# Performance work log

Measured on AMD Instinct MI355X. Metric: run time of the kernel, lower is better.

The kernel has to match this reference:

```python
import jax, jax.numpy as jnp
import numpy as np

N = 20000      # nodes
E = 640000     # edges (avg degree 32)
H = 128        # hidden_channels
L = 12         # num_layers
DIN = 3        # node feature dim
DE = 4         # edge feature dim
DOUT = 16      # output dim (y_s size)
EPS = 1e-7     # GENConv message eps
LN_EPS = 1e-5


def setup_inputs() -> dict:
    key = jax.random.key(0)
    ks = jax.random.split(key, 12)

    def w(k, shape, fan_in):
        return (jax.random.normal(k, shape, dtype=jnp.float32) / np.float32(np.sqrt(fan_in)))

    return {
        "x": jax.random.normal(ks[0], (N, DIN), dtype=jnp.float32),
        "edge_index": jax.random.randint(ks[1], (2, E), 0, N, dtype=jnp.int32),
        "edge_attr": jax.random.uniform(ks[2], (E, DE), dtype=jnp.float32),
        "enc_node_w": w(ks[3], (DIN, H), DIN),
        "enc_node_b": jnp.zeros((H,), jnp.float32),
        "enc_edge_w": w(ks[4], (DE, H), DE),
        "enc_edge_b": jnp.zeros((H,), jnp.float32),
        "t": jnp.ones((L,), jnp.float32),                 # learnable softmax temperature per layer
        "mlp1_w": w(ks[5], (L, H, 2 * H), H),
        "mlp1_b": jnp.zeros((L, 2 * H), jnp.float32),
        "mlp_ln_g": jnp.ones((L, 2 * H), jnp.float32),
        "mlp_ln_b": jnp.zeros((L, 2 * H), jnp.float32),
        "mlp2_w": w(ks[6], (L, 2 * H, H), 2 * H),
        "mlp2_b": jnp.zeros((L, H), jnp.float32),
        "ln_g": jnp.ones((L, H), jnp.float32),            # DeepGCNLayer pre-norm params
        "ln_b": jnp.zeros((L, H), jnp.float32),
        "lin_w": w(ks[7], (H, DOUT), H),
        "lin_b": jnp.zeros((DOUT,), jnp.float32),
    }


def _layer_norm(x, g, b):
    mu = jnp.mean(x, axis=-1, keepdims=True)
    var = jnp.mean(jnp.square(x - mu), axis=-1, keepdims=True)
    return (x - mu) * jax.lax.rsqrt(var + LN_EPS) * g + b


def _genconv(h, src, dst, ea, ti, w1, b1, g1, bb1, w2, b2):
    # message: relu(x_j + edge_attr) + eps  -> [E, H]
    m = jax.nn.relu(h[src] + ea) + EPS
    # learnable-temperature softmax over edges grouped by destination node
    logits = m * ti
    mx = jax.ops.segment_max(logits, dst, num_segments=N)
    mx = jnp.where(jnp.isfinite(mx), mx, 0.0)  # guard empty segments
    ex = jnp.exp(logits - mx[dst])
    den = jax.ops.segment_sum(ex, dst, num_segments=N) + 1e-16
    agg = jax.ops.segment_sum(m * (ex / den[dst]), dst, num_segments=N)
    # GENConv update: out = MLP(agg + x) with MLP = Lin(H,2H)->LN->ReLU->Lin(2H,H)
    out = agg + h
    u = jax.nn.relu(_layer_norm(out @ w1 + b1, g1, bb1))
    return u @ w2 + b2


def reference(x, edge_index, edge_attr, enc_node_w, enc_node_b, enc_edge_w,
              enc_edge_b, t, mlp1_w, mlp1_b, mlp_ln_g, mlp_ln_b, mlp2_w,
              mlp2_b, ln_g, ln_b, lin_w, lin_b):
    src, dst = edge_index[0], edge_index[1]
    h = x @ enc_node_w + enc_node_b            # node encoder
    ea = edge_attr @ enc_edge_w + enc_edge_b   # edge encoder

    # first layer: conv only (no norm/act, no residual)
    h = _genconv(h, src, dst, ea, t[0], mlp1_w[0], mlp1_b[0], mlp_ln_g[0],
                 mlp_ln_b[0], mlp2_w[0], mlp2_b[0])

    # remaining layers: res+ block  x = x + conv(relu(norm(x)))
    for i in range(1, L):
        hn = jax.nn.relu(_layer_norm(h, ln_g[i], ln_b[i]))
        h = h + _genconv(hn, src, dst, ea, t[i], mlp1_w[i], mlp1_b[i],
                         mlp_ln_g[i], mlp_ln_b[i], mlp2_w[i], mlp2_b[i])

    # final: layers[0].act(layers[0].norm(x)) then output linear
    h = jax.nn.relu(_layer_norm(h, ln_g[0], ln_b[0]))
    return h @ lin_w + lin_b
```

## Files before the change

### kernel.cpp

```cpp
#include <hip/hip_runtime.h>
#include <hip/hip_bf16.h>
#include <math.h>

#define NN 20000
#define EE 640000
#define HH 128
#define LL 12
#define DOUT_ 16
#define EPS_ 1e-7f
#define LN_EPS_ 1e-5f

typedef unsigned short u16;
typedef unsigned int u32;
typedef __attribute__((ext_vector_type(8))) short bf16x8;
typedef __attribute__((ext_vector_type(4))) float f32x4;

__device__ inline u16 bf16_rne(float v) {
  u32 u = __float_as_uint(v);
  return (u16)((u + 0x7FFFu + ((u >> 16) & 1u)) >> 16);
}
__device__ inline float bf16_tof(u16 h) { return __uint_as_float(((u32)h) << 16); }

__global__ __launch_bounds__(256) void hist_kernel(const int* __restrict__ dst, int* __restrict__ deg) {
  int e = blockIdx.x * 256 + threadIdx.x;
  if (e < EE) atomicAdd(&deg[dst[e]], 1);
}

__global__ __launch_bounds__(1024) void scan_kernel(const int* __restrict__ deg, int* __restrict__ off,
                                                    int* __restrict__ cur) {
  __shared__ int part[1024];
  int tid = threadIdx.x;
  const int CH = (NN + 1023) >> 10;
  int base = tid * CH;
  int s = 0;
  for (int j = 0; j < CH; ++j) { int i = base + j; if (i < NN) s += deg[i]; }
  part[tid] = s;
  __syncthreads();
  for (int d = 1; d < 1024; d <<= 1) {
    int v = (tid >= d) ? part[tid - d] : 0;
    __syncthreads();
    part[tid] += v;
    __syncthreads();
  }
  int run = part[tid] - s;
  for (int j = 0; j < CH; ++j) {
    int i = base + j;
    if (i < NN) { off[i] = run; cur[i] = run; run += deg[i]; }
  }
  if (tid == 1023) off[NN] = part[1023];
}

__global__ __launch_bounds__(256) void scatter_kernel(const int* __restrict__ src, const int* __restrict__ dst,
                                                      const float4* __restrict__ ea, int* __restrict__ cur,
                                                      int* __restrict__ srcs, float4* __restrict__ ea4) {
  int e = blockIdx.x * 256 + threadIdx.x;
  if (e >= EE) return;
  int d = dst[e];
  int p = atomicAdd(&cur[d], 1);
  srcs[p] = src[e];
  ea4[p] = ea[e];
}

__global__ __launch_bounds__(256) void wpack_kernel(const float* __restrict__ w, u16* __restrict__ dh,
                                                    int K, int N, int KSC) {
  int fid = blockIdx.x * 256 + threadIdx.x;
  int perL = (K * N) >> 3;
  if (fid >= LL * perL) return;
  int l = fid / perL, r = fid % perL;
  int lane = r & 63;
  int r2 = r >> 6;
  int ks2 = r2 % KSC; r2 /= KSC;
  int NT = N >> 4;
  int tI = r2 % NT;
  int chunk = r2 / NT;
  int c16 = lane & 15, kg = lane >> 4;
  int n = tI * 16 + c16;
  int k0 = (chunk * KSC + ks2) * 32 + kg * 8;
  const float* ws = w + (size_t)l * K * N;
  u16* oh = dh + (size_t)fid * 8;
  #pragma unroll
  for (int j = 0; j < 8; ++j) {
    oh[j] = bf16_rne(ws[(size_t)(k0 + j) * N + n]);
  }
}

__global__ __launch_bounds__(256) void encoder_kernel(const float* __restrict__ x, const float* __restrict__ w,
                                                      const float* __restrict__ b, float* __restrict__ h,
                                                      u16* __restrict__ hb) {
  int id = blockIdx.x * 256 + threadIdx.x;
  if (id >= NN * 64) return;
  int n = id >> 6, cp = id & 63;
  int c0 = cp * 2;
  float x0 = x[n*3+0], x1 = x[n*3+1], x2 = x[n*3+2];
  float vx = b[c0]   + x0*w[c0]   + x1*w[HH+c0]   + x2*w[2*HH+c0];
  float vy = b[c0+1] + x0*w[c0+1] + x1*w[HH+c0+1] + x2*w[2*HH+c0+1];
  *(float2*)&h[(size_t)n*HH + c0] = make_float2(vx, vy);
  *(u32*)&hb[(size_t)n*HH + c0] = (u32)bf16_rne(vx) | ((u32)bf16_rne(vy) << 16);
}

__global__ __launch_bounds__(256) void conv_kernel(const float* __restrict__ hn,
                                                   const u16* __restrict__ hb,
                                                   const int* __restrict__ off,
                                                   const int* __restrict__ srcs, const float4* __restrict__ ea4,
                                                   const float* __restrict__ eew, const float* __restrict__ eeb,
                                                   const float* __restrict__ t, int layer,
                                                   u16* __restrict__ tmpH, u16* __restrict__ tmpL) {
  int wid = blockIdx.x * 4 + (threadIdx.x >> 6);
  int lane = threadIdx.x & 63;
  if (wid >= NN) return;
  int c0 = lane * 2;
  float ti = t[layer];
  float w0x = eew[c0],      w0y = eew[c0+1];
  float w1x = eew[HH+c0],   w1y = eew[HH+c0+1];
  float w2x = eew[2*HH+c0], w2y = eew[2*HH+c0+1];
  float w3x = eew[3*HH+c0], w3y = eew[3*HH+c0+1];
  float bx = eeb[c0], by = eeb[c0+1];
  int e0 = off[wid], e1 = off[wid+1];
  float2 hd = *(const float2*)&hn[(size_t)wid*HH + c0];
  float den0 = 0.f, den1 = 0.f, num0 = 0.f, num1 = 0.f;

  int e = e0;
  const int UF = 8;
  for (; e + UF <= e1; e += UF) {
    int si[UF]; float4 av[UF];
    #pragma unroll
    for (int u = 0; u < UF; ++u) { si[u] = srcs[e + u]; av[u] = ea4[e + u]; }
    u32 hv[UF];
    #pragma unroll
    for (int u = 0; u < UF; ++u) hv[u] = *(const u32*)&hb[((u32)si[u] << 7) + c0];
    #pragma unroll
    for (int u = 0; u < UF; ++u) {
      float hx = bf16_tof((u16)(hv[u] & 0xffffu));
      float hy = bf16_tof((u16)(hv[u] >> 16));
      float eax = fmaf(av[u].w, w3x, fmaf(av[u].z, w2x, fmaf(av[u].y, w1x, fmaf(av[u].x, w0x, bx))));
      float eay = fmaf(av[u].w, w3y, fmaf(av[u].z, w2y, fmaf(av[u].y, w1y, fmaf(av[u].x, w0y, by))));
      float m0 = fmaxf(hx + eax, 0.f) + EPS_;
      float m1 = fmaxf(hy + eay, 0.f) + EPS_;
      float p0 = __expf(m0 * ti);
      float p1 = __expf(m1 * ti);
      den0 += p0; den1 += p1;
      num0 = fmaf(m0, p0, num0);
      num1 = fmaf(m1, p1, num1);
    }
  }
  for (; e < e1; ++e) {
    int sidx = srcs[e];
    float4 a = ea4[e];
    u32 hv = *(const u32*)&hb[((u32)sidx << 7) + c0];
    float hx = bf16_tof((u16)(hv & 0xffffu));
    float hy = bf16_tof((u16)(hv >> 16));
    float eax = fmaf(a.w, w3x, fmaf(a.z, w2x, fmaf(a.y, w1x, fmaf(a.x, w0x, bx))));
    float eay = fmaf(a.w, w3y, fmaf(a.z, w2y, fmaf(a.y, w1y, fmaf(a.x, w0y, by))));
    float m0 = fmaxf(hx + eax, 0.f) + EPS_;
    float m1 = fmaxf(hy + eay, 0.f) + EPS_;
    float p0 = __expf(m0 * ti);
    float p1 = __expf(m1 * ti);
    den0 += p0; den1 += p1;
    num0 = fmaf(m0, p0, num0);
    num1 = fmaf(m1, p1, num1);
  }
  float v0 = num0 / (den0 + 1e-16f) + hd.x;
  float v1 = num1 / (den1 + 1e-16f) + hd.y;
  u16 h0 = bf16_rne(v0), h1 = bf16_rne(v1);
  u16 l0 = bf16_rne(v0 - bf16_tof(h0)), l1 = bf16_rne(v1 - bf16_tof(h1));
  *(u32*)&tmpH[(size_t)wid*HH + c0] = (u32)h0 | ((u32)h1 << 16);
  *(u32*)&tmpL[(size_t)wid*HH + c0] = (u32)l0 | ((u32)l1 << 16);
}

__global__ __launch_bounds__(256) void mlp_fused(const u16* __restrict__ Ah, const u16* __restrict__ Al,
                                                 const u16* __restrict__ B1h,
                                                 const float* __restrict__ b1,
                                                 const float* __restrict__ g1, const float* __restrict__ bb1,
                                                 const u16* __restrict__ B2h,
                                                 const float* __restrict__ b2,
                                                 const float* __restrict__ gn, const float* __restrict__ bn,
                                                 float* __restrict__ h, float* __restrict__ hnb,
                                                 u16* __restrict__ hb, int first) {
  __shared__ u16 Us[16][264];
  __shared__ float red[4][16][2];
  int tid = threadIdx.x;
  int wv = tid >> 6, lane = tid & 63;
  int c16 = lane & 15, kg = lane >> 4;
  int row0 = blockIdx.x * 16;

  const u16* pAh = Ah + (size_t)(row0 + c16) * HH + kg * 8;
  const u16* pAl = Al + (size_t)(row0 + c16) * HH + kg * 8;
  bf16x8 ah[4], al[4];
  #pragma unroll
  for (int ks = 0; ks < 4; ++ks) {
    ah[ks] = *(const bf16x8*)(pAh + ks * 32);
    al[ks] = *(const bf16x8*)(pAl + ks * 32);
  }
  f32x4 acc[4];
  #pragma unroll
  for (int i = 0; i < 4; ++i) acc[i] = (f32x4){0.f, 0.f, 0.f, 0.f};
  #pragma unroll
  for (int ch = 0; ch < 4; ++ch) {
    #pragma unroll
    for (int i = 0; i < 4; ++i) {
      int tI = wv * 4 + i;
      size_t boff = ((size_t)(ch * 16 + tI) * 64 + lane) * 8;
      bf16x8 bh = *(const bf16x8*)&B1h[boff];
      acc[i] = __builtin_amdgcn_mfma_f32_16x16x32_bf16(ah[ch], bh, acc[i], 0, 0, 0);
      acc[i] = __builtin_amdgcn_mfma_f32_16x16x32_bf16(al[ch], bh, acc[i], 0, 0, 0);
    }
  }
  {
    float bv[4], gv[4], bbv[4];
    #pragma unroll
    for (int i = 0; i < 4; ++i) {
      int c = (wv * 4 + i) * 16 + c16;
      bv[i] = b1[c]; gv[i] = g1[c]; bbv[i] = bb1[c];
    }
    float xv[4][4], s1[4], s2[4];
    #pragma unroll
    for (int j = 0; j < 4; ++j) {
      float a1 = 0.f, a2 = 0.f;
      #pragma unroll
      for (int i = 0; i < 4; ++i) {
        float v = acc[i][j] + bv[i];
        xv[j][i] = v; a1 += v; a2 = fmaf(v, v, a2);
      }
      #pragma unroll
      for (int m = 1; m <= 8; m <<= 1) { a1 += __shfl_xor(a1, m); a2 += __shfl_xor(a2, m); }
      s1[j] = a1; s2[j] = a2;
    }
    if (c16 == 0) {
      #pragma unroll
      for (int j = 0; j < 4; ++j) { red[wv][kg*4+j][0] = s1[j]; red[wv][kg*4+j][1] = s2[j]; }
    }
    __syncthreads();
    #pragma unroll
    for (int j = 0; j < 4; ++j) {
      int row = kg * 4 + j;
      float S1 = red[0][row][0] + red[1][row][0] + red[2][row][0] + red[3][row][0];
      float S2 = red[0][row][1] + red[1][row][1] + red[2][row][1] + red[3][row][1];
      float mu = S1 * (1.f / 256.f);
      float var = fmaxf(S2 * (1.f / 256.f) - mu * mu, 0.f);
      float rs = rsqrtf(var + LN_EPS_);
      #pragma unroll
      for (int i = 0; i < 4; ++i) {
        float o = fmaxf((xv[j][i] - mu) * rs * gv[i] + bbv[i], 0.f);
        Us[row][(wv * 4 + i) * 16 + c16] = bf16_rne(o);
      }
    }
  }
  __syncthreads();

  bf16x8 ua[8];
  #pragma unroll
  for (int ks = 0; ks < 8; ++ks) ua[ks] = *(const bf16x8*)&Us[c16][ks * 32 + kg * 8];
  f32x4 acc2[2];
  #pragma unroll
  for (int i = 0; i < 2; ++i) acc2[i] = (f32x4){0.f, 0.f, 0.f, 0.f};
  #pragma unroll
  for (int ch = 0; ch < 4; ++ch) {
    #pragma unroll
    for (int ks2 = 0; ks2 < 2; ++ks2) {
      int ks = ch * 2 + ks2;
      #pragma unroll
      for (int i = 0; i < 2; ++i) {
        int tI = wv * 2 + i;
        size_t boff = ((size_t)(ch * 16 + tI * 2 + ks2) * 64 + lane) * 8;
        bf16x8 bh = *(const bf16x8*)&B2h[boff];
        acc2[i] = __builtin_amdgcn_mfma_f32_16x16x32_bf16(ua[ks], bh, acc2[i], 0, 0, 0);
      }
    }
  }
  {
    float bv[2], gv[2], bnv[2];
    #pragma unroll
    for (int i = 0; i < 2; ++i) {
      int c = (wv * 2 + i) * 16 + c16;
      bv[i] = b2[c]; gv[i] = gn[c]; bnv[i] = bn[c];
    }
    float xv[4][2], s1[4], s2[4];
    #pragma unroll
    for (int j = 0; j < 4; ++j) {
      int row = row0 + kg * 4 + j;
      float a1 = 0.f, a2 = 0.f;
      #pragma unroll
      for (int i = 0; i < 2; ++i) {
        size_t p = (size_t)row * HH + (wv * 2 + i) * 16 + c16;
        float v = acc2[i][j] + bv[i];
        if (!first) v += h[p];
        xv[j][i] = v;
        h[p] = v;
        a1 += v; a2 = fmaf(v, v, a2);
      }
      #pragma unroll
      for (int m = 1; m <= 8; m <<= 1) { a1 += __shfl_xor(a1, m); a2 += __shfl_xor(a2, m); }
      s1[j] = a1; s2[j] = a2;
    }
    if (c16 == 0) {
      #pragma unroll
      for (int j = 0; j < 4; ++j) { red[wv][kg*4+j][0] = s1[j]; red[wv][kg*4+j][1] = s2[j]; }
    }
    __syncthreads();
    #pragma unroll
    for (int j = 0; j < 4; ++j) {
      int row = kg * 4 + j;
      float S1 = red[0][row][0] + red[1][row][0] + red[2][row][0] + red[3][row][0];
      float S2 = red[0][row][1] + red[1][row][1] + red[2][row][1] + red[3][row][1];
      float mu = S1 * (1.f / 128.f);
      float var = fmaxf(S2 * (1.f / 128.f) - mu * mu, 0.f);
      float rs = rsqrtf(var + LN_EPS_);
      #pragma unroll
      for (int i = 0; i < 2; ++i) {
        float o = fmaxf((xv[j][i] - mu) * rs * gv[i] + bnv[i], 0.f);
        size_t p = (size_t)(row0 + row) * HH + (wv * 2 + i) * 16 + c16;
        hnb[p] = o;
        hb[p] = bf16_rne(o);
      }
    }
  }
}

__global__ __launch_bounds__(256) void outgemm_kernel(const float* __restrict__ hn, const float* __restrict__ w,
                                                      const float* __restrict__ b, float* __restrict__ out) {
  __shared__ float Ws[HH * DOUT_];
  int tid = threadIdx.x;
  {
    const float4* s4 = (const float4*)w;
    float4* d4 = (float4*)Ws;
    d4[tid*2] = s4[tid*2]; d4[tid*2+1] = s4[tid*2+1];
  }
  __syncthreads();
  int id = blockIdx.x * 256 + tid;
  int n = id >> 4, c = id & 15;
  if (n >= NN) return;
  float s = b[c];
  const float* hr = &hn[(size_t)n*HH];
  #pragma unroll 8
  for (int k = 0; k < HH; ++k) s += hr[k] * Ws[k*DOUT_ + c];
  out[n*DOUT_ + c] = s;
}

extern "C" void kernel_launch(void* const* d_in, const int* in_sizes, int n_in,
                              void* d_out, int out_size, void* d_ws, size_t ws_size,
                              hipStream_t stream) {
  const float* x    = (const float*)d_in[0];
  const int*   ei   = (const int*)d_in[1];
  const float* eatt = (const float*)d_in[2];
  const float* enw  = (const float*)d_in[3];
  const float* enb  = (const float*)d_in[4];
  const float* eew  = (const float*)d_in[5];
  const float* eeb  = (const float*)d_in[6];
  const float* t    = (const float*)d_in[7];
  const float* m1w  = (const float*)d_in[8];
  const float* m1b  = (const float*)d_in[9];
  const float* mlg  = (const float*)d_in[10];
  const float* mlb  = (const float*)d_in[11];
  const float* m2w  = (const float*)d_in[12];
  const float* m2b  = (const float*)d_in[13];
  const float* lng  = (const float*)d_in[14];
  const float* lnb  = (const float*)d_in[15];
  const float* linw = (const float*)d_in[16];
  const float* linb = (const float*)d_in[17];
  float* out = (float*)d_out;

  char* ws = (char*)d_ws;
  size_t o = 0;
  auto take = [&](size_t bytes) { char* p = ws + o; o = (o + bytes + 255) & ~(size_t)255; return p; };
  int*    deg  = (int*)take((size_t)NN * 4);
  int*    off  = (int*)take((size_t)(NN + 1) * 4);
  int*    cur  = (int*)take((size_t)NN * 4);
  int*    srcs = (int*)take((size_t)EE * 4);
  float4* ea4  = (float4*)take((size_t)EE * 16);
  float*  h    = (float*)take((size_t)NN * HH * 4);
  float*  hnb  = (float*)take((size_t)NN * HH * 4);
  u16*    hb   = (u16*)take((size_t)NN * HH * 2);
  u16*    tmpH = (u16*)take((size_t)NN * HH * 2);
  u16*    tmpL = (u16*)take((size_t)NN * HH * 2);
  u16*    w1h  = (u16*)take((size_t)LL * HH * 256 * 2);
  u16*    w2h  = (u16*)take((size_t)LL * 256 * HH * 2);

  const int* src = ei;
  const int* dst = ei + EE;

  hipMemsetAsync(deg, 0, (size_t)NN * 4, stream);
  hist_kernel<<<(EE + 255) / 256, 256, 0, stream>>>(dst, deg);
  scan_kernel<<<1, 1024, 0, stream>>>(deg, off, cur);
  scatter_kernel<<<(EE + 255) / 256, 256, 0, stream>>>(src, dst, (const float4*)eatt, cur, srcs, ea4);
  int wblocks = (LL * HH * 256 / 8 + 255) / 256;
  wpack_kernel<<<wblocks, 256, 0, stream>>>(m1w, w1h, HH, 256, 1);
  wpack_kernel<<<wblocks, 256, 0, stream>>>(m2w, w2h, 256, HH, 2);
  encoder_kernel<<<(NN * 64 + 255) / 256, 256, 0, stream>>>(x, enw, enb, h, hb);

  int gblocks = NN / 16;
  for (int i = 0; i < LL; ++i) {
    const float* cin = (i == 0) ? h : hnb;
    conv_kernel<<<(NN + 3) / 4, 256, 0, stream>>>(cin, hb, off, srcs, ea4, eew, eeb, t, i, tmpH, tmpL);
    int nrm = (i + 1) % LL;
    mlp_fused<<<gblocks, 256, 0, stream>>>(tmpH, tmpL,
                                           w1h + (size_t)i * 32768,
                                           m1b + i * 256, mlg + i * 256, mlb + i * 256,
                                           w2h + (size_t)i * 32768,
                                           m2b + i * HH, lng + nrm * HH, lnb + nrm * HH,
                                           h, hnb, hb, i == 0 ? 1 : 0);
  }
  outgemm_kernel<<<(NN * DOUT_ + 255) / 256, 256, 0, stream>>>(hnb, linw, linb, out);
}
```

Before: 844.1 us.

## Process 32 rows per block in fused MLP to reuse weight fragments

The fused MLP kernel now handles two 16-row tiles per block, so every weight fragment loaded from global memory feeds two MFMA chains instead of one. This halves weight traffic per row and the number of blocks, 625 instead of 1250. In exchange it raises register and LDS use per block and leaves fewer blocks to spread across the GPU. NN=20000 divides by 32, so no tail handling is needed.

```diff
diff --git a/kernel.cpp b/kernel.cpp
--- a/kernel.cpp
+++ b/kernel.cpp
@@ -176,33 +176,33 @@
                                                  const float* __restrict__ gn, const float* __restrict__ bn,
                                                  float* __restrict__ h, float* __restrict__ hnb,
                                                  u16* __restrict__ hb, int first) {
-  __shared__ u16 Us[16][264];
-  __shared__ float red[4][16][2];
+  __shared__ u16 Us[32][264];
+  __shared__ float red[4][32][2];
   int tid = threadIdx.x;
   int wv = tid >> 6, lane = tid & 63;
   int c16 = lane & 15, kg = lane >> 4;
-  int row0 = blockIdx.x * 16;
-
-  const u16* pAh = Ah + (size_t)(row0 + c16) * HH + kg * 8;
-  const u16* pAl = Al + (size_t)(row0 + c16) * HH + kg * 8;
-  bf16x8 ah[4], al[4];
+  int row0 = blockIdx.x * 32;
+
+  f32x4 acc[2][4];
   #pragma unroll
-  for (int ks = 0; ks < 4; ++ks) {
-    ah[ks] = *(const bf16x8*)(pAh + ks * 32);
-    al[ks] = *(const bf16x8*)(pAl + ks * 32);
-  }
-  f32x4 acc[4];
-  #pragma unroll
-  for (int i = 0; i < 4; ++i) acc[i] = (f32x4){0.f, 0.f, 0.f, 0.f};
+  for (int rt = 0; rt < 2; ++rt)
+    #pragma unroll
+    for (int i = 0; i < 4; ++i) acc[rt][i] = (f32x4){0.f, 0.f, 0.f, 0.f};
   #pragma unroll
   for (int ch = 0; ch < 4; ++ch) {
+    bf16x8 a0h = *(const bf16x8*)(Ah + (size_t)(row0 + c16) * HH + ch * 32 + kg * 8);
+    bf16x8 a0l = *(const bf16x8*)(Al + (size_t)(row0 + c16) * HH + ch * 32 + kg * 8);
+    bf16x8 a1h = *(const bf16x8*)(Ah + (size_t)(row0 + 16 + c16) * HH + ch * 32 + kg * 8);
+    bf16x8 a1l = *(const bf16x8*)(Al + (size_t)(row0 + 16 + c16) * HH + ch * 32 + kg * 8);
     #pragma unroll
     for (int i = 0; i < 4; ++i) {
       int tI = wv * 4 + i;
       size_t boff = ((size_t)(ch * 16 + tI) * 64 + lane) * 8;
       bf16x8 bh = *(const bf16x8*)&B1h[boff];
-      acc[i] = __builtin_amdgcn_mfma_f32_16x16x32_bf16(ah[ch], bh, acc[i], 0, 0, 0);
-      acc[i] = __builtin_amdgcn_mfma_f32_16x16x32_bf16(al[ch], bh, acc[i], 0, 0, 0);
+      acc[0][i] = __builtin_amdgcn_mfma_f32_16x16x32_bf16(a0h, bh, acc[0][i], 0, 0, 0);
+      acc[0][i] = __builtin_amdgcn_mfma_f32_16x16x32_bf16(a0l, bh, acc[0][i], 0, 0, 0);
+      acc[1][i] = __builtin_amdgcn_mfma_f32_16x16x32_bf16(a1h, bh, acc[1][i], 0, 0, 0);
+      acc[1][i] = __builtin_amdgcn_mfma_f32_16x16x32_bf16(a1l, bh, acc[1][i], 0, 0, 0);
     }
   }
   {
@@ -212,58 +212,62 @@
       int c = (wv * 4 + i) * 16 + c16;
       bv[i] = b1[c]; gv[i] = g1[c]; bbv[i] = bb1[c];
     }
-    float xv[4][4], s1[4], s2[4];
-    #pragma unroll
-    for (int j = 0; j < 4; ++j) {
-      float a1 = 0.f, a2 = 0.f;
+    float xv[2][4][4];
+    #pragma unroll
+    for (int rt = 0; rt < 2; ++rt) {
       #pragma unroll
-      for (int i = 0; i < 4; ++i) {
-        float v = acc[i][j] + bv[i];
-        xv[j][i] = v; a1 += v; a2 = fmaf(v, v, a2);
+      for (int j = 0; j < 4; ++j) {
+        float a1 = 0.f, a2 = 0.f;
+        #pragma unroll
+        for (int i = 0; i < 4; ++i) {
+          float v = acc[rt][i][j] + bv[i];
+          xv[rt][j][i] = v; a1 += v; a2 = fmaf(v, v, a2);
+        }
+        #pragma unroll
+        for (int m = 1; m <= 8; m <<= 1) { a1 += __shfl_xor(a1, m); a2 += __shfl_xor(a2, m); }
+        if (c16 == 0) { red[wv][rt*16 + kg*4 + j][0] = a1; red[wv][rt*16 + kg*4 + j][1] = a2; }
       }
+    }
+    __syncthreads();
+    #pragma unroll
+    for (int rt = 0; rt < 2; ++rt) {
       #pragma unroll
-      for (int m = 1; m <= 8; m <<= 1) { a1 += __shfl_xor(a1, m); a2 += __shfl_xor(a2, m); }
-      s1[j] = a1; s2[j] = a2;
-    }
-    if (c16 == 0) {
-      #pragma unroll
-      for (int j = 0; j < 4; ++j) { red[wv][kg*4+j][0] = s1[j]; red[wv][kg*4+j][1] = s2[j]; }
-    }
-    __syncthreads();
-    #pragma unroll
-    for (int j = 0; j < 4; ++j) {
-      int row = kg * 4 + j;
-      float S1 = red[0][row][0] + red[1][row][0] + red[2][row][0] + red[3][row][0];
-      float S2 = red[0][row][1] + red[1][row][1] + red[2][row][1] + red[3][row][1];
-      float mu = S1 * (1.f / 256.f);
-      float var = fmaxf(S2 * (1.f / 256.f) - mu * mu, 0.f);
-      float rs = rsqrtf(var + LN_EPS_);
-      #pragma unroll
-      for (int i = 0; i < 4; ++i) {
-        float o = fmaxf((xv[j][i] - mu) * rs * gv[i] + bbv[i], 0.f);
-        Us[row][(wv * 4 + i) * 16 + c16] = bf16_rne(o);
+      for (int j = 0; j < 4; ++j) {
+        int row = rt * 16 + kg * 4 + j;
+        float S1 = red[0][row][0] + red[1][row][0] + red[2][row][0] + red[3][row][0];
+        float S2 = red[0][row][1] + red[1][row][1] + red[2][row][1] + red[3][row][1];
+        float mu = S1 * (1.f / 256.f);
+        float var = fmaxf(S2 * (1.f / 256.f) - mu * mu, 0.f);
+        float rs = rsqrtf(var + LN_EPS_);
+        #pragma unroll
+        for (int i = 0; i < 4; ++i) {
+          float o = fmaxf((xv[rt][j][i] - mu) * rs * gv[i] + bbv[i], 0.f);
+          Us[row][(wv * 4 + i) * 16 + c16] = bf16_rne(o);
+        }
       }
     }
   }
   __syncthreads();
 
-  bf16x8 ua[8];
+  f32x4 acc2[2][2];
   #pragma unroll
-  for (int ks = 0; ks < 8; ++ks) ua[ks] = *(const bf16x8*)&Us[c16][ks * 32 + kg * 8];
-  f32x4 acc2[2];
-  #pragma unroll
-  for (int i = 0; i < 2; ++i) acc2[i] = (f32x4){0.f, 0.f, 0.f, 0.f};
+  for (int rt = 0; rt < 2; ++rt)
+    #pragma unroll
+    for (int i = 0; i < 2; ++i) acc2[rt][i] = (f32x4){0.f, 0.f, 0.f, 0.f};
   #pragma unroll
   for (int ch = 0; ch < 4; ++ch) {
     #pragma unroll
     for (int ks2 = 0; ks2 < 2; ++ks2) {
       int ks = ch * 2 + ks2;
+      bf16x8 u0 = *(const bf16x8*)&Us[c16][ks * 32 + kg * 8];
+      bf16x8 u1 = *(const bf16x8*)&Us[16 + c16][ks * 32 + kg * 8];
       #pragma unroll
       for (int i = 0; i < 2; ++i) {
         int tI = wv * 2 + i;
         size_t boff = ((size_t)(ch * 16 + tI * 2 + ks2) * 64 + lane) * 8;
         bf16x8 bh = *(const bf16x8*)&B2h[boff];
-        acc2[i] = __builtin_amdgcn_mfma_f32_16x16x32_bf16(ua[ks], bh, acc2[i], 0, 0, 0);
+        acc2[0][i] = __builtin_amdgcn_mfma_f32_16x16x32_bf16(u0, bh, acc2[0][i], 0, 0, 0);
+        acc2[1][i] = __builtin_amdgcn_mfma_f32_16x16x32_bf16(u1, bh, acc2[1][i], 0, 0, 0);
       }
     }
   }
@@ -274,43 +278,45 @@
       int c = (wv * 2 + i) * 16 + c16;
       bv[i] = b2[c]; gv[i] = gn[c]; bnv[i] = bn[c];
     }
-    float xv[4][2], s1[4], s2[4];
-    #pragma unroll
-    for (int j = 0; j < 4; ++j) {
-      int row = row0 + kg * 4 + j;
-      float a1 = 0.f, a2 = 0.f;
+    float xv[2][4][2];
+    #pragma unroll
+    for (int rt = 0; rt < 2; ++rt) {
       #pragma unroll
-      for (int i = 0; i < 2; ++i) {
-        size_t p = (size_t)row * HH + (wv * 2 + i) * 16 + c16;
-        float v = acc2[i][j] + bv[i];
-        if (!first) v += h[p];
-        xv[j][i] = v;
-        h[p] = v;
-        a1 += v; a2 = fmaf(v, v, a2);
+      for (int j = 0; j < 4; ++j) {
+        int row = row0 + rt * 16 + kg * 4 + j;
+        float a1 = 0.f, a2 = 0.f;
+        #pragma unroll
+        for (int i = 0; i < 2; ++i) {
+          size_t p = (size_t)row * HH + (wv * 2 + i) * 16 + c16;
+          float v = acc2[rt][i][j] + bv[i];
+          if (!first) v += h[p];
+          xv[rt][j][i] = v;
+          h[p] = v;
+          a1 += v; a2 = fmaf(v, v, a2);
+        }
+        #pragma unroll
+        for (int m = 1; m <= 8; m <<= 1) { a1 += __shfl_xor(a1, m); a2 += __shfl_xor(a2, m); }
+        if (c16 == 0) { red[wv][rt*16 + kg*4 + j][0] = a1; red[wv][rt*16 + kg*4 + j][1] = a2; }
       }
+    }
+    __syncthreads();
+    #pragma unroll
+    for (int rt = 0; rt < 2; ++rt) {
       #pragma unroll
-      for (int m = 1; m <= 8; m <<= 1) { a1 += __shfl_xor(a1, m); a2 += __shfl_xor(a2, m); }
-      s1[j] = a1; s2[j] = a2;
-    }
-    if (c16 == 0) {
-      #pragma unroll
-      for (int j = 0; j < 4; ++j) { red[wv][kg*4+j][0] = s1[j]; red[wv][kg*4+j][1] = s2[j]; }
-    }
-    __syncthreads();
-    #pragma unroll
-    for (int j = 0; j < 4; ++j) {
-      int row = kg * 4 + j;
-      float S1 = red[0][row][0] + red[1][row][0] + red[2][row][0] + red[3][row][0];
-      float S2 = red[0][row][1] + red[1][row][1] + red[2][row][1] + red[3][row][1];
-      float mu = S1 * (1.f / 128.f);
-      float var = fmaxf(S2 * (1.f / 128.f) - mu * mu, 0.f);
-      float rs = rsqrtf(var + LN_EPS_);
-      #pragma unroll
-      for (int i = 0; i < 2; ++i) {
-        float o = fmaxf((xv[j][i] - mu) * rs * gv[i] + bnv[i], 0.f);
-        size_t p = (size_t)(row0 + row) * HH + (wv * 2 + i) * 16 + c16;
-        hnb[p] = o;
-        hb[p] = bf16_rne(o);
+      for (int j = 0; j < 4; ++j) {
+        int row = rt * 16 + kg * 4 + j;
+        float S1 = red[0][row][0] + red[1][row][0] + red[2][row][0] + red[3][row][0];
+        float S2 = red[0][row][1] + red[1][row][1] + red[2][row][1] + red[3][row][1];
+        float mu = S1 * (1.f / 128.f);
+        float var = fmaxf(S2 * (1.f / 128.f) - mu * mu, 0.f);
+        float rs = rsqrtf(var + LN_EPS_);
+        #pragma unroll
+        for (int i = 0; i < 2; ++i) {
+          float o = fmaxf((xv[rt][j][i] - mu) * rs * gv[i] + bnv[i], 0.f);
+          size_t p = (size_t)(row0 + row) * HH + (wv * 2 + i) * 16 + c16;
+          hnb[p] = o;
+          hb[p] = bf16_rne(o);
+        }
       }
     }
   }
@@ -387,7 +393,7 @@
   wpack_kernel<<<wblocks, 256, 0, stream>>>(m2w, w2h, 256, HH, 2);
   encoder_kernel<<<(NN * 64 + 255) / 256, 256, 0, stream>>>(x, enw, enb, h, hb);
 
-  int gblocks = NN / 16;
+  int gblocks = NN / 32;
   for (int i = 0; i < LL; ++i) {
     const float* cin = (i == 0) ? h : hnb;
     conv_kernel<<<(NN + 3) / 4, 256, 0, stream>>>(cin, hb, off, srcs, ea4, eew, eeb, t, i, tmpH, tmpL);
```

Measured after the change: 886.4 us. +5.0%, slower.
